# Performance work log

Measured on AMD Instinct MI355X. Metric: run time of the kernel, lower is better.

The kernel has to match this reference:

```python
import jax, jax.numpy as jnp
import numpy as np

STRIDE = 14
C_LOCAL = 2
NUM_HEADS = 12


def sparse_attention_mask(n_tokens, stride_length=STRIDE, c=C_LOCAL, mode='fixed'):
    q = jnp.arange(n_tokens)[:, None]  # row index Q
    k = jnp.arange(n_tokens)[None, :]  # col index K
    if mode == 'fixed':
        m1 = (q // stride_length) == (k // stride_length)
        m2 = ((k % stride_length) >= stride_length - c) & ((k % stride_length) <= stride_length)
        return m1 | m2
    elif mode == 'strided':
        m1 = jnp.abs(q - k) <= stride_length
        m2 = ((q - k) % stride_length) == 0
        return m1 | m2


def setup_inputs() -> dict:
    key = jax.random.key(0)
    ks = jax.random.split(key, 5)
    B, N, C = 16, 1024, 768
    return {
        'x': jax.random.normal(ks[0], (B, N, C), dtype=jnp.float32),
        'w_qkv': jax.random.normal(ks[1], (3 * C, C), dtype=jnp.float32) * (1.0 / np.sqrt(C)),
        'b_qkv': jax.random.normal(ks[2], (3 * C,), dtype=jnp.float32) * 0.02,
        'w_proj': jax.random.normal(ks[3], (C, C), dtype=jnp.float32) * (1.0 / np.sqrt(C)),
        'b_proj': jax.random.normal(ks[4], (C,), dtype=jnp.float32) * 0.02,
    }


def reference(x, w_qkv, b_qkv, w_proj, b_proj):
    B, N, C = x.shape
    H = NUM_HEADS
    D = C // H
    mask = sparse_attention_mask(N, mode='fixed')  # [N, N] bool

    # qkv projection: [B,N,3C] -> [3,B,H,N,D]
    qkv = x @ w_qkv.T + b_qkv
    qkv = qkv.reshape(B, N, 3, H, D).transpose(2, 0, 3, 1, 4)
    q, k, v = qkv[0], qkv[1], qkv[2]

    # SDPA with default scale = 1/sqrt(head_dim) and boolean attn_mask
    scale = 1.0 / jnp.sqrt(jnp.asarray(D, dtype=x.dtype))
    scores = jnp.einsum('bhnd,bhmd->bhnm', q, k) * scale
    scores = jnp.where(mask[None, None, :, :], scores, jnp.finfo(scores.dtype).min)
    attn = jax.nn.softmax(scores, axis=-1)
    out = jnp.einsum('bhnm,bhmd->bhnd', attn, v)

    # merge heads and output projection
    out = out.transpose(0, 2, 1, 3).reshape(B, N, C)
    return out @ w_proj.T + b_proj
```

## Files before the change

### kernel.cpp

```cpp
#include <hip/hip_runtime.h>
#include <stdint.h>

typedef unsigned short u16;
typedef __attribute__((ext_vector_type(8))) short bf16x8;
typedef __attribute__((ext_vector_type(4))) short s16x4;
typedef __attribute__((ext_vector_type(4))) float f32x4;

__device__ __forceinline__ u16 f2bf(float f) {
  uint32_t x = __builtin_bit_cast(uint32_t, f);
  uint32_t r = (x + 0x7fffu + ((x >> 16) & 1u)) >> 16;
  return (u16)r;
}
__device__ __forceinline__ float bf2f(u16 u) {
  return __builtin_bit_cast(float, (uint32_t)u << 16);
}

typedef __attribute__((address_space(3))) uint32_t lds_u32;
typedef const __attribute__((address_space(1))) uint32_t glb_u32;
__device__ __forceinline__ void gload_lds16(const void* g, void* l) {
  __builtin_amdgcn_global_load_lds(
      reinterpret_cast<glb_u32*>(reinterpret_cast<uintptr_t>(g)),
      reinterpret_cast<lds_u32*>(reinterpret_cast<uintptr_t>(l)),
      16, 0, 0);
}

__device__ __forceinline__ int swz(int r) { return (r & 3) ^ ((r >> 2) & 3); }

__global__ void cvt_split_kernel(const float* __restrict__ in, u16* __restrict__ hi,
                                 u16* __restrict__ lo, int n4) {
  typedef __attribute__((ext_vector_type(4))) float float4v;
  int i = blockIdx.x * 256 + threadIdx.x;
  const int stride = gridDim.x * 256;
  for (; i < n4; i += stride) {
    float4v v = *(const float4v*)(in + (size_t)i * 4);
    s16x4 hv;
#pragma unroll
    for (int j = 0; j < 4; ++j) hv[j] = (short)f2bf(v[j]);
    *(s16x4*)(hi + (size_t)i * 4) = hv;
    if (lo) {
      s16x4 lv;
#pragma unroll
      for (int j = 0; j < 4; ++j) lv[j] = (short)f2bf(v[j] - bf2f((u16)hv[j]));
      *(s16x4*)(lo + (size_t)i * 4) = lv;
    }
  }
}

template <int OUTF32>
__global__ __launch_bounds__(512, 2) void gemm_bt2(
    const u16* __restrict__ A, const u16* __restrict__ B0,
    const float* __restrict__ bias, float* __restrict__ outF, u16* __restrict__ outB,
    int Ndim, int Kdim) {
  __shared__ u16 sA[3][256 * 32];
  __shared__ u16 sB[3][256 * 32];

  const int tid = threadIdx.x;
  const int lane = tid & 63;
  const int wid = tid >> 6;
  const int wr = wid >> 2;
  const int wc = wid & 3;
  const int brow = blockIdx.x * 256;
  const int bcol = blockIdx.y * 256;
  const int colL = lane & 15;
  const int kgrp = lane >> 4;
  const int NT = Kdim >> 5;

  int srcA[2], srcB[2], ldsU[2];
#pragma unroll
  for (int j = 0; j < 2; ++j) {
    const int u = (wid * 2 + j) * 64 + lane;
    const int r = u >> 2;
    const int sl = (u & 3) ^ swz(r);
    srcA[j] = (brow + r) * Kdim + sl * 8;
    srcB[j] = (bcol + r) * Kdim + sl * 8;
    ldsU[j] = u * 8;
  }

  int oa[8], ob[4];
#pragma unroll
  for (int m = 0; m < 8; ++m) {
    const int r = wr * 128 + m * 16 + colL;
    oa[m] = r * 32 + ((kgrp ^ swz(r)) * 8);
  }
#pragma unroll
  for (int n = 0; n < 4; ++n) {
    const int r = wc * 64 + n * 16 + colL;
    ob[n] = r * 32 + ((kgrp ^ swz(r)) * 8);
  }

  auto stage = [&](int buf, int t) {
    const int k0 = t << 5;
#pragma unroll
    for (int j = 0; j < 2; ++j) {
      gload_lds16(A + (size_t)(srcA[j] + k0), &sA[buf][ldsU[j]]);
      gload_lds16(B0 + (size_t)(srcB[j] + k0), &sB[buf][ldsU[j]]);
    }
  };

  f32x4 acc[8][4] = {};

  stage(0, 0);
  stage(1, 1);
  asm volatile("s_waitcnt vmcnt(4)" ::: "memory");
  __builtin_amdgcn_s_barrier();

  for (int t = 0; t < NT; ++t) {
    const int cur = t % 3;
    if (t + 2 < NT) stage((t + 2) % 3, t + 2);

    bf16x8 a[8], b[4];
#pragma unroll
    for (int m = 0; m < 8; ++m) a[m] = *(const bf16x8*)&sA[cur][oa[m]];
#pragma unroll
    for (int n = 0; n < 4; ++n) b[n] = *(const bf16x8*)&sB[cur][ob[n]];

    __builtin_amdgcn_s_setprio(1);
#pragma unroll
    for (int m = 0; m < 8; ++m)
#pragma unroll
      for (int n = 0; n < 4; ++n)
        acc[m][n] = __builtin_amdgcn_mfma_f32_16x16x32_bf16(a[m], b[n], acc[m][n], 0, 0, 0);
    __builtin_amdgcn_s_setprio(0);

    if (t + 2 < NT)
      asm volatile("s_waitcnt vmcnt(4)" ::: "memory");
    else
      asm volatile("s_waitcnt vmcnt(0)" ::: "memory");
    __builtin_amdgcn_s_barrier();
  }

  const int r0 = kgrp * 4;
#pragma unroll
  for (int n = 0; n < 4; ++n) {
    const int colg = bcol + wc * 64 + n * 16 + colL;
    const float bv = bias[colg];
#pragma unroll
    for (int m = 0; m < 8; ++m) {
      const int rowg = brow + wr * 128 + m * 16 + r0;
#pragma unroll
      for (int r = 0; r < 4; ++r) {
        const float v = acc[m][n][r] + bv;
        if (OUTF32)
          outF[(size_t)(rowg + r) * Ndim + colg] = v;
        else
          outB[(size_t)(rowg + r) * Ndim + colg] = f2bf(v);
      }
    }
  }
}

__global__ __launch_bounds__(256) void transpose_v_kernel(const u16* __restrict__ qkv,
                                                          u16* __restrict__ vt) {
  __shared__ u16 t[64][72];
  const int tid = threadIdx.x;
  const int nt = blockIdx.x, h = blockIdx.y, b = blockIdx.z;
  const u16* src = qkv + (size_t)(b * 1024 + nt * 64) * 2304 + 1536 + h * 64;
#pragma unroll
  for (int j = 0; j < 2; ++j) {
    const int c = j * 256 + tid;
    const int row = c >> 3;
    const int off = (c & 7) * 8;
    *(bf16x8*)&t[row][off] = *(const bf16x8*)(src + (size_t)row * 2304 + off);
  }
  __syncthreads();
  u16* dst = vt + (size_t)(b * 12 + h) * 64 * 1024 + nt * 64;
#pragma unroll
  for (int j = 0; j < 2; ++j) {
    const int c = j * 256 + tid;
    const int drow = c >> 3;
    const int noff = (c & 7) * 8;
    bf16x8 o;
#pragma unroll
    for (int i = 0; i < 8; ++i) o[i] = (short)t[noff + i][drow];
    *(bf16x8*)(dst + (size_t)drow * 1024 + noff) = o;
  }
}

__global__ __launch_bounds__(256) void gather_global_kernel(const u16* __restrict__ qkv,
                                                            u16* __restrict__ kgc,
                                                            u16* __restrict__ vgc) {
  __shared__ u16 tl[192][72];
  const int tid = threadIdx.x;
  const int h = blockIdx.x % 12;
  const int b = blockIdx.x / 12;
  const u16* Kg = qkv + (size_t)(b * 1024) * 2304 + 768 + h * 64;
  const u16* Vg = qkv + (size_t)(b * 1024) * 2304 + 1536 + h * 64;
  u16* kout = kgc + (size_t)blockIdx.x * 192 * 64;
  u16* vout = vgc + (size_t)blockIdx.x * 64 * 192;

  for (int t = tid; t < 1536; t += 256) {
    const int s = t >> 3, ch = t & 7;
    bf16x8 kv = {}, vv = {};
    if (s < 146) {
      const int tok = (s >> 1) * 14 + 12 + (s & 1);
      kv = *(const bf16x8*)(Kg + (size_t)tok * 2304 + ch * 8);
      vv = *(const bf16x8*)(Vg + (size_t)tok * 2304 + ch * 8);
    }
    *(bf16x8*)(kout + s * 64 + ch * 8) = kv;
    *(bf16x8*)&tl[s][ch * 8] = vv;
  }
  __syncthreads();
  for (int t = tid; t < 64 * 24; t += 256) {
    const int d = t / 24, c8 = (t % 24) * 8;
    bf16x8 o;
#pragma unroll
    for (int i = 0; i < 8; ++i) o[i] = (short)tl[c8 + i][d];
    *(bf16x8*)(vout + (size_t)d * 192 + c8) = o;
  }
}

__global__ __launch_bounds__(256, 2) void attn_kernel(const u16* __restrict__ qkv,
                                                      const u16* __restrict__ vt,
                                                      const u16* __restrict__ kgc,
                                                      const u16* __restrict__ vgc,
                                                      u16* __restrict__ ao) {
  __shared__ u16 sQ[64 * 64];
  __shared__ u16 sK[2][64 * 64];
  __shared__ u16 sV[2][64 * 64];
  __shared__ u16 sP[4][16 * 72];

  const int tid = threadIdx.x;
  const int lane = tid & 63;
  const int wid = tid >> 6;
  const int qt = blockIdx.x, h = blockIdx.y, b = blockIdx.z;
  const int q0 = qt * 64;
  const int colL = lane & 15;
  const int kgrp = lane >> 4;
  const int bh = b * 12 + h;

  const u16* Qg = qkv + (size_t)(b * 1024 + q0) * 2304 + h * 64;
  const u16* Kg = qkv + (size_t)(b * 1024) * 2304 + 768 + h * 64;
  const u16* Vt = vt + (size_t)bh * 64 * 1024;
  const u16* Kc = kgc + (size_t)bh * 192 * 64;
  const u16* Vc = vgc + (size_t)bh * 64 * 192;

  const int first_blk = q0 / 14;
  const int tok0a = (first_blk * 14) & ~7;

  auto stage_kv = [&](int buf, int it) {
    if (it < 3) {
#pragma unroll
      for (int j = 0; j < 2; ++j) {
        const int c = j * 256 + tid;
        const int row = c >> 3;
        const int sb = ((c & 7) * 16) ^ ((row & 7) << 4);
        gload_lds16((const char*)(Kc + (size_t)(it * 64 + row) * 64) + sb, &sK[buf][c * 8]);
        gload_lds16((const char*)(Vc + (size_t)row * 192 + it * 64) + sb, &sV[buf][c * 8]);
      }
    } else {
      const int tc0 = tok0a + (it - 3) * 64;
#pragma unroll
      for (int j = 0; j < 2; ++j) {
        const int c = j * 256 + tid;
        const int row = c >> 3;
        const int sb = ((c & 7) * 16) ^ ((row & 7) << 4);
        const int ktok = min(tc0 + row, 1023);
        gload_lds16((const char*)(Kg + (size_t)ktok * 2304) + sb, &sK[buf][c * 8]);
        const int vb = min(tc0 * 2 + sb, 2032);
        gload_lds16((const char*)(Vt + (size_t)row * 1024) + vb, &sV[buf][c * 8]);
      }
    }
  };

#pragma unroll
  for (int j = 0; j < 2; ++j) {
    const int c = j * 256 + tid;
    const int row = c >> 3;
    const int off = (c & 7) * 8;
    gload_lds16(Qg + (size_t)row * 2304 + off, &sQ[c * 8]);
  }
  stage_kv(0, 0);
  __syncthreads();

  bf16x8 qf[2];
#pragma unroll
  for (int ks = 0; ks < 2; ++ks)
    qf[ks] = *(const bf16x8*)&sQ[(wid * 16 + colL) * 64 + ks * 32 + kgrp * 8];

  int qblk[4];
#pragma unroll
  for (int r = 0; r < 4; ++r) qblk[r] = (q0 + wid * 16 + kgrp * 4 + r) / 14;

  const float SCL = 0.125f * 1.44269504088896f;
  const float NEG = -3e38f;
  float mrun[4] = {NEG, NEG, NEG, NEG};
  float lsum[4] = {0.f, 0.f, 0.f, 0.f};
  f32x4 oacc[4] = {};

  for (int it = 0; it < 5; ++it) {
    const int cur = it & 1;
    if (it + 1 < 5) stage_kv(cur ^ 1, it + 1);

    f32x4 s[4] = {};
#pragma unroll
    for (int n = 0; n < 4; ++n) {
      const int row = n * 16 + colL;
#pragma unroll
      for (int ks = 0; ks < 2; ++ks) {
        const int cb = (ks * 32 + kgrp * 8) * 2;
        bf16x8 kf = *(const bf16x8*)((const char*)&sK[cur][0] + row * 128 + (cb ^ ((row & 7) << 4)));
        s[n] = __builtin_amdgcn_mfma_f32_16x16x32_bf16(qf[ks], kf, s[n], 0, 0, 0);
      }
    }

    float sv[4][4];
    if (it < 3) {
#pragma unroll
      for (int n = 0; n < 4; ++n) {
        const bool gv = (it * 64 + n * 16 + colL) < 146;
#pragma unroll
        for (int r = 0; r < 4; ++r) sv[n][r] = gv ? s[n][r] * SCL : NEG;
      }
    } else {
      const int tc0 = tok0a + (it - 3) * 64;
#pragma unroll
      for (int n = 0; n < 4; ++n) {
        const int t = tc0 + n * 16 + colL;
        const int tb = t / 14;
        const bool cv = (t < 1024) && ((t - tb * 14) < 12);
#pragma unroll
        for (int r = 0; r < 4; ++r) {
          const bool ok = cv && (tb == qblk[r]);
          sv[n][r] = ok ? s[n][r] * SCL : NEG;
        }
      }
    }

    float pmax[4];
#pragma unroll
    for (int r = 0; r < 4; ++r) {
      float v = fmaxf(fmaxf(sv[0][r], sv[1][r]), fmaxf(sv[2][r], sv[3][r]));
#pragma unroll
      for (int msk = 1; msk <= 8; msk <<= 1) v = fmaxf(v, __shfl_xor(v, msk));
      pmax[r] = v;
    }

    float corr[4], psum[4];
#pragma unroll
    for (int r = 0; r < 4; ++r) {
      const float mn = fmaxf(mrun[r], pmax[r]);
      corr[r] = exp2f(mrun[r] - mn);
      mrun[r] = mn;
      psum[r] = 0.f;
    }

    float p[4][4];
#pragma unroll
    for (int n = 0; n < 4; ++n)
#pragma unroll
      for (int r = 0; r < 4; ++r) {
        p[n][r] = exp2f(sv[n][r] - mrun[r]);
        psum[r] += p[n][r];
      }

#pragma unroll
    for (int r = 0; r < 4; ++r) {
      float v = psum[r];
#pragma unroll
      for (int msk = 1; msk <= 8; msk <<= 1) v += __shfl_xor(v, msk);
      lsum[r] = lsum[r] * corr[r] + v;
    }

#pragma unroll
    for (int n = 0; n < 4; ++n)
#pragma unroll
      for (int r = 0; r < 4; ++r)
        sP[wid][(kgrp * 4 + r) * 72 + n * 16 + colL] = f2bf(p[n][r]);

#pragma unroll
    for (int dn = 0; dn < 4; ++dn)
#pragma unroll
      for (int r = 0; r < 4; ++r) oacc[dn][r] *= corr[r];

#pragma unroll
    for (int ks = 0; ks < 2; ++ks) {
      bf16x8 pf = *(const bf16x8*)&sP[wid][colL * 72 + ks * 32 + kgrp * 8];
#pragma unroll
      for (int dn = 0; dn < 4; ++dn) {
        const int vrow = dn * 16 + colL;
        const int cb = (ks * 32 + kgrp * 8) * 2;
        bf16x8 vf = *(const bf16x8*)((const char*)&sV[cur][0] + vrow * 128 + (cb ^ ((vrow & 7) << 4)));
        oacc[dn] = __builtin_amdgcn_mfma_f32_16x16x32_bf16(pf, vf, oacc[dn], 0, 0, 0);
      }
    }

    __syncthreads();
  }

  float inv[4];
#pragma unroll
  for (int r = 0; r < 4; ++r) inv[r] = 1.0f / lsum[r];
#pragma unroll
  for (int dn = 0; dn < 4; ++dn)
#pragma unroll
    for (int r = 0; r < 4; ++r) {
      const int rowg = b * 1024 + q0 + wid * 16 + kgrp * 4 + r;
      const int colg = h * 64 + dn * 16 + colL;
      ao[(size_t)rowg * 768 + colg] = f2bf(oacc[dn][r] * inv[r]);
    }
}

extern "C" void kernel_launch(void* const* d_in, const int* in_sizes, int n_in,
                              void* d_out, int out_size, void* d_ws, size_t ws_size,
                              hipStream_t stream) {
  const float* x = (const float*)d_in[0];
  const float* w_qkv = (const float*)d_in[1];
  const float* b_qkv = (const float*)d_in[2];
  const float* w_proj = (const float*)d_in[3];
  const float* b_proj = (const float*)d_in[4];
  float* out = (float*)d_out;

  char* ws = (char*)d_ws;
  size_t off = 0;
  auto alloc = [&](size_t bytes) {
    char* p = ws + off;
    off += (bytes + 255) & ~(size_t)255;
    return p;
  };
  u16* x_bf = (u16*)alloc(16384ull * 768 * 2);
  u16* wq_bf = (u16*)alloc(2304ull * 768 * 2);
  u16* wp_bf = (u16*)alloc(768ull * 768 * 2);
  u16* qkvb = (u16*)alloc(16384ull * 2304 * 2);
  u16* vt = (u16*)alloc(192ull * 64 * 1024 * 2);
  u16* kgc = (u16*)alloc(192ull * 192 * 64 * 2);
  u16* vgc = (u16*)alloc(192ull * 64 * 192 * 2);
  u16* ao = x_bf;

  cvt_split_kernel<<<dim3(4096), dim3(256), 0, stream>>>(x, x_bf, nullptr, 16384 * 768 / 4);
  cvt_split_kernel<<<dim3(1728), dim3(256), 0, stream>>>(w_qkv, wq_bf, nullptr, 2304 * 768 / 4);
  cvt_split_kernel<<<dim3(576), dim3(256), 0, stream>>>(w_proj, wp_bf, nullptr, 768 * 768 / 4);

  gemm_bt2<0><<<dim3(64, 9), dim3(512), 0, stream>>>(x_bf, wq_bf, b_qkv,
                                                     nullptr, qkvb, 2304, 768);
  transpose_v_kernel<<<dim3(16, 12, 16), dim3(256), 0, stream>>>(qkvb, vt);
  gather_global_kernel<<<dim3(192), dim3(256), 0, stream>>>(qkvb, kgc, vgc);
  attn_kernel<<<dim3(16, 12, 16), dim3(256), 0, stream>>>(qkvb, vt, kgc, vgc, ao);
  gemm_bt2<1><<<dim3(64, 3), dim3(512), 0, stream>>>(ao, wp_bf, b_proj,
                                                     out, nullptr, 768, 768);
}
```

Measured before the change: 221.8 us.

## Restructure GEMM into 8-phase pipelined schedule with K=64 tiles and double buffering

Rewrites the bf16 GEMM main loop to use 64-wide K tiles with two LDS buffers instead of three 32-wide buffers. Each K-step is split into four quadrant phases, and the A/B prefetches for step t+2 are interleaved between MFMA blocks so global loads overlap compute. The LDS swizzle changes to an XOR over 8 slots, and launch bounds drop to one block per SM because LDS use doubles to 128KB. The extra barriers per iteration and the lower occupancy could offset the better overlap.

Result: faster. 210.8 us (-5.0%).

```diff
diff --git a/kernel.cpp b/kernel.cpp
--- a/kernel.cpp
+++ b/kernel.cpp
@@ -23,8 +23,6 @@
       reinterpret_cast<lds_u32*>(reinterpret_cast<uintptr_t>(l)),
       16, 0, 0);
 }
-
-__device__ __forceinline__ int swz(int r) { return (r & 3) ^ ((r >> 2) & 3); }
 
 __global__ void cvt_split_kernel(const float* __restrict__ in, u16* __restrict__ hi,
                                  u16* __restrict__ lo, int n4) {
@@ -47,12 +45,12 @@
 }
 
 template <int OUTF32>
-__global__ __launch_bounds__(512, 2) void gemm_bt2(
+__global__ __launch_bounds__(512, 1) void gemm_8p(
     const u16* __restrict__ A, const u16* __restrict__ B0,
     const float* __restrict__ bias, float* __restrict__ outF, u16* __restrict__ outB,
     int Ndim, int Kdim) {
-  __shared__ u16 sA[3][256 * 32];
-  __shared__ u16 sB[3][256 * 32];
+  __shared__ u16 sA[2][256 * 64];
+  __shared__ u16 sB[2][256 * 64];
 
   const int tid = threadIdx.x;
   const int lane = tid & 63;
@@ -63,70 +61,137 @@
   const int bcol = blockIdx.y * 256;
   const int colL = lane & 15;
   const int kgrp = lane >> 4;
-  const int NT = Kdim >> 5;
-
-  int srcA[2], srcB[2], ldsU[2];
-#pragma unroll
-  for (int j = 0; j < 2; ++j) {
-    const int u = (wid * 2 + j) * 64 + lane;
-    const int r = u >> 2;
-    const int sl = (u & 3) ^ swz(r);
-    srcA[j] = (brow + r) * Kdim + sl * 8;
-    srcB[j] = (bcol + r) * Kdim + sl * 8;
-    ldsU[j] = u * 8;
-  }
-
-  int oa[8], ob[4];
+  const int NT = Kdim >> 6;
+
+  int srcA[4], srcB[4], ldsOff[4];
+#pragma unroll
+  for (int j = 0; j < 4; ++j) {
+    const int u = j * 512 + tid;
+    const int r = u >> 3;
+    const int s = u & 7;
+    const int sp = (s ^ (r & 7)) * 8;
+    srcA[j] = (brow + r) * Kdim + sp;
+    srcB[j] = (bcol + r) * Kdim + sp;
+    ldsOff[j] = u * 8;
+  }
+
+  int offA[8][2], offB[4][2];
 #pragma unroll
   for (int m = 0; m < 8; ++m) {
     const int r = wr * 128 + m * 16 + colL;
-    oa[m] = r * 32 + ((kgrp ^ swz(r)) * 8);
+#pragma unroll
+    for (int kk = 0; kk < 2; ++kk)
+      offA[m][kk] = r * 64 + ((kk * 32 + kgrp * 8) ^ ((r & 7) << 3));
   }
 #pragma unroll
   for (int n = 0; n < 4; ++n) {
     const int r = wc * 64 + n * 16 + colL;
-    ob[n] = r * 32 + ((kgrp ^ swz(r)) * 8);
-  }
-
-  auto stage = [&](int buf, int t) {
-    const int k0 = t << 5;
-#pragma unroll
-    for (int j = 0; j < 2; ++j) {
-      gload_lds16(A + (size_t)(srcA[j] + k0), &sA[buf][ldsU[j]]);
-      gload_lds16(B0 + (size_t)(srcB[j] + k0), &sB[buf][ldsU[j]]);
-    }
+#pragma unroll
+    for (int kk = 0; kk < 2; ++kk)
+      offB[n][kk] = r * 64 + ((kk * 32 + kgrp * 8) ^ ((r & 7) << 3));
+  }
+
+  auto stageA = [&](int slot, int kt) {
+    const int k0 = kt << 6;
+#pragma unroll
+    for (int j = 0; j < 4; ++j)
+      gload_lds16(A + (size_t)(srcA[j] + k0), &sA[slot][ldsOff[j]]);
   };
+  auto stageB = [&](int slot, int kt) {
+    const int k0 = kt << 6;
+#pragma unroll
+    for (int j = 0; j < 4; ++j)
+      gload_lds16(B0 + (size_t)(srcB[j] + k0), &sB[slot][ldsOff[j]]);
+  };
 
   f32x4 acc[8][4] = {};
 
-  stage(0, 0);
-  stage(1, 1);
-  asm volatile("s_waitcnt vmcnt(4)" ::: "memory");
-  __builtin_amdgcn_s_barrier();
+  stageA(0, 0);
+  stageB(0, 0);
+  if (NT > 1) {
+    stageA(1, 1);
+    stageB(1, 1);
+    asm volatile("s_waitcnt vmcnt(8)" ::: "memory");
+  } else {
+    asm volatile("s_waitcnt vmcnt(0)" ::: "memory");
+  }
+  asm volatile("s_barrier" ::: "memory");
 
   for (int t = 0; t < NT; ++t) {
-    const int cur = t % 3;
-    if (t + 2 < NT) stage((t + 2) % 3, t + 2);
-
-    bf16x8 a[8], b[4];
-#pragma unroll
-    for (int m = 0; m < 8; ++m) a[m] = *(const bf16x8*)&sA[cur][oa[m]];
-#pragma unroll
-    for (int n = 0; n < 4; ++n) b[n] = *(const bf16x8*)&sB[cur][ob[n]];
-
+    const int d = t & 1;
+    bf16x8 a0[4][2], a1[4][2], b0[2][2], b1[2][2];
+
+#pragma unroll
+    for (int m = 0; m < 4; ++m)
+#pragma unroll
+      for (int kk = 0; kk < 2; ++kk) a0[m][kk] = *(const bf16x8*)&sA[d][offA[m][kk]];
+#pragma unroll
+    for (int n = 0; n < 2; ++n)
+#pragma unroll
+      for (int kk = 0; kk < 2; ++kk) b0[n][kk] = *(const bf16x8*)&sB[d][offB[n][kk]];
+    asm volatile("s_waitcnt lgkmcnt(0)" ::: "memory");
+    __builtin_amdgcn_sched_barrier(0);
     __builtin_amdgcn_s_setprio(1);
 #pragma unroll
-    for (int m = 0; m < 8; ++m)
-#pragma unroll
-      for (int n = 0; n < 4; ++n)
-        acc[m][n] = __builtin_amdgcn_mfma_f32_16x16x32_bf16(a[m], b[n], acc[m][n], 0, 0, 0);
+    for (int m = 0; m < 4; ++m)
+#pragma unroll
+      for (int n = 0; n < 2; ++n)
+#pragma unroll
+        for (int kk = 0; kk < 2; ++kk)
+          acc[m][n] = __builtin_amdgcn_mfma_f32_16x16x32_bf16(a0[m][kk], b0[n][kk], acc[m][n], 0, 0, 0);
     __builtin_amdgcn_s_setprio(0);
-
+    asm volatile("s_barrier" ::: "memory");
+
+#pragma unroll
+    for (int n = 0; n < 2; ++n)
+#pragma unroll
+      for (int kk = 0; kk < 2; ++kk) b1[n][kk] = *(const bf16x8*)&sB[d][offB[n + 2][kk]];
+    asm volatile("s_waitcnt lgkmcnt(0)" ::: "memory");
+    __builtin_amdgcn_sched_barrier(0);
+    __builtin_amdgcn_s_setprio(1);
+#pragma unroll
+    for (int m = 0; m < 4; ++m)
+#pragma unroll
+      for (int n = 0; n < 2; ++n)
+#pragma unroll
+        for (int kk = 0; kk < 2; ++kk)
+          acc[m][n + 2] = __builtin_amdgcn_mfma_f32_16x16x32_bf16(a0[m][kk], b1[n][kk], acc[m][n + 2], 0, 0, 0);
+    __builtin_amdgcn_s_setprio(0);
+    asm volatile("s_barrier" ::: "memory");
+
+#pragma unroll
+    for (int m = 0; m < 4; ++m)
+#pragma unroll
+      for (int kk = 0; kk < 2; ++kk) a1[m][kk] = *(const bf16x8*)&sA[d][offA[m + 4][kk]];
+    asm volatile("s_waitcnt lgkmcnt(0)" ::: "memory");
+    __builtin_amdgcn_sched_barrier(0);
+    if (t + 2 < NT) stageB(d, t + 2);
+    __builtin_amdgcn_s_setprio(1);
+#pragma unroll
+    for (int m = 0; m < 4; ++m)
+#pragma unroll
+      for (int n = 0; n < 2; ++n)
+#pragma unroll
+        for (int kk = 0; kk < 2; ++kk)
+          acc[m + 4][n + 2] = __builtin_amdgcn_mfma_f32_16x16x32_bf16(a1[m][kk], b1[n][kk], acc[m + 4][n + 2], 0, 0, 0);
+    __builtin_amdgcn_s_setprio(0);
+    asm volatile("s_barrier" ::: "memory");
+
+    if (t + 2 < NT) stageA(d, t + 2);
+    __builtin_amdgcn_s_setprio(1);
+#pragma unroll
+    for (int m = 0; m < 4; ++m)
+#pragma unroll
+      for (int n = 0; n < 2; ++n)
+#pragma unroll
+        for (int kk = 0; kk < 2; ++kk)
+          acc[m + 4][n] = __builtin_amdgcn_mfma_f32_16x16x32_bf16(a1[m][kk], b0[n][kk], acc[m + 4][n], 0, 0, 0);
+    __builtin_amdgcn_s_setprio(0);
     if (t + 2 < NT)
-      asm volatile("s_waitcnt vmcnt(4)" ::: "memory");
-    else
+      asm volatile("s_waitcnt vmcnt(8)" ::: "memory");
+    else if (t + 1 < NT)
       asm volatile("s_waitcnt vmcnt(0)" ::: "memory");
-    __builtin_amdgcn_s_barrier();
+    asm volatile("s_barrier" ::: "memory");
   }
 
   const int r0 = kgrp * 4;
@@ -430,11 +495,11 @@
   cvt_split_kernel<<<dim3(1728), dim3(256), 0, stream>>>(w_qkv, wq_bf, nullptr, 2304 * 768 / 4);
   cvt_split_kernel<<<dim3(576), dim3(256), 0, stream>>>(w_proj, wp_bf, nullptr, 768 * 768 / 4);
 
-  gemm_bt2<0><<<dim3(64, 9), dim3(512), 0, stream>>>(x_bf, wq_bf, b_qkv,
-                                                     nullptr, qkvb, 2304, 768);
+  gemm_8p<0><<<dim3(64, 9), dim3(512), 0, stream>>>(x_bf, wq_bf, b_qkv,
+                                                    nullptr, qkvb, 2304, 768);
   transpose_v_kernel<<<dim3(16, 12, 16), dim3(256), 0, stream>>>(qkvb, vt);
   gather_global_kernel<<<dim3(192), dim3(256), 0, stream>>>(qkvb, kgc, vgc);
   attn_kernel<<<dim3(16, 12, 16), dim3(256), 0, stream>>>(qkvb, vt, kgc, vgc, ao);
-  gemm_bt2<1><<<dim3(64, 3), dim3(512), 0, stream>>>(ao, wp_bf, b_proj,
-                                                     out, nullptr, 768, 768);
-}
+  gemm_8p<1><<<dim3(64, 3), dim3(512), 0, stream>>>(ao, wp_bf, b_proj,
+                                                    out, nullptr, 768, 768);
+}
```

## Replace GEMM tiling with full-K A-resident row-panel kernel streaming B panels

Applied to the files above, without the earlier changes.

Both projection GEMMs now use a kernel where each block loads a 64x768 slab of A fully into LDS once and streams all output-column panels of B through a triple-buffered pipeline. Results are written out after each 256-wide panel. The launch grows from 576 or 192 blocks to 256 blocks, which evens out the wave count across CUs. The intent is to avoid re-reading A for every column tile and to balance work. The cost is much larger LDS use (occupancy 1 block per CU), a smaller per-wave MFMA tile (2x4 instead of 8x4) with more B traffic, and K fixed at 768.

Result: slower. 238.4 us (+7.5%).

```diff
diff --git a/kernel.cpp b/kernel.cpp
--- a/kernel.cpp
+++ b/kernel.cpp
@@ -24,7 +24,7 @@
       16, 0, 0);
 }
 
-__device__ __forceinline__ int swz(int r) { return (r & 3) ^ ((r >> 2) & 3); }
+__device__ __forceinline__ int swzB(int r) { return (r & 3) ^ ((r >> 2) & 3); }
 
 __global__ void cvt_split_kernel(const float* __restrict__ in, u16* __restrict__ hi,
                                  u16* __restrict__ lo, int n4) {
@@ -46,12 +46,11 @@
   }
 }
 
-template <int OUTF32>
-__global__ __launch_bounds__(512, 2) void gemm_bt2(
+template <int OUTF32, int NPAN>
+__global__ __launch_bounds__(512, 1) void gemm_sn(
     const u16* __restrict__ A, const u16* __restrict__ B0,
-    const float* __restrict__ bias, float* __restrict__ outF, u16* __restrict__ outB,
-    int Ndim, int Kdim) {
-  __shared__ u16 sA[3][256 * 32];
+    const float* __restrict__ bias, float* __restrict__ outF, u16* __restrict__ outB) {
+  __shared__ u16 sA[64 * 768];
   __shared__ u16 sB[3][256 * 32];
 
   const int tid = threadIdx.x;
@@ -59,93 +58,105 @@
   const int wid = tid >> 6;
   const int wr = wid >> 2;
   const int wc = wid & 3;
-  const int brow = blockIdx.x * 256;
-  const int bcol = blockIdx.y * 256;
+  const int brow = blockIdx.x * 64;
   const int colL = lane & 15;
   const int kgrp = lane >> 4;
-  const int NT = Kdim >> 5;
-
-  int srcA[2], srcB[2], ldsU[2];
+  const int Ndim = NPAN * 256;
+  const int G = NPAN * 24;
+
+  int srcA[12];
+#pragma unroll
+  for (int j = 0; j < 12; ++j) {
+    const int u = j * 512 + tid;
+    const int r = u / 96;
+    const int s = u % 96;
+    srcA[j] = (brow + r) * 768 + ((s ^ (r & 7)) * 8);
+  }
+
+  int rowB[2], ldsB[2];
 #pragma unroll
   for (int j = 0; j < 2; ++j) {
-    const int u = (wid * 2 + j) * 64 + lane;
+    const int u = j * 512 + tid;
     const int r = u >> 2;
-    const int sl = (u & 3) ^ swz(r);
-    srcA[j] = (brow + r) * Kdim + sl * 8;
-    srcB[j] = (bcol + r) * Kdim + sl * 8;
-    ldsU[j] = u * 8;
-  }
-
-  int oa[8], ob[4];
-#pragma unroll
-  for (int m = 0; m < 8; ++m) {
-    const int r = wr * 128 + m * 16 + colL;
-    oa[m] = r * 32 + ((kgrp ^ swz(r)) * 8);
-  }
-#pragma unroll
-  for (int n = 0; n < 4; ++n) {
-    const int r = wc * 64 + n * 16 + colL;
-    ob[n] = r * 32 + ((kgrp ^ swz(r)) * 8);
-  }
-
-  auto stage = [&](int buf, int t) {
-    const int k0 = t << 5;
-#pragma unroll
-    for (int j = 0; j < 2; ++j) {
-      gload_lds16(A + (size_t)(srcA[j] + k0), &sA[buf][ldsU[j]]);
-      gload_lds16(B0 + (size_t)(srcB[j] + k0), &sB[buf][ldsU[j]]);
-    }
+    const int s = u & 3;
+    rowB[j] = r * 768 + ((s ^ swzB(r)) * 8);
+    ldsB[j] = u * 8;
+  }
+
+  const int ax = colL & 7;
+  int baseA[2];
+#pragma unroll
+  for (int m = 0; m < 2; ++m) baseA[m] = (wr * 32 + m * 16 + colL) * 768;
+  const int slotB = kgrp ^ swzB(colL);
+  int offB[4];
+#pragma unroll
+  for (int n = 0; n < 4; ++n) offB[n] = (wc * 64 + n * 16 + colL) * 32 + slotB * 8;
+
+  auto stageB = [&](int slot, int g) {
+    const int pan = g / 24, t = g % 24;
+    const int base = pan * (256 * 768) + t * 32;
+#pragma unroll
+    for (int j = 0; j < 2; ++j)
+      gload_lds16(B0 + (size_t)(rowB[j] + base), &sB[slot][ldsB[j]]);
   };
 
-  f32x4 acc[8][4] = {};
-
-  stage(0, 0);
-  stage(1, 1);
-  asm volatile("s_waitcnt vmcnt(4)" ::: "memory");
+#pragma unroll
+  for (int j = 0; j < 12; ++j)
+    gload_lds16(A + (size_t)srcA[j], &sA[(size_t)(j * 512 + tid) * 8]);
+  stageB(0, 0);
+  if (G > 1) stageB(1, 1);
+  asm volatile("s_waitcnt vmcnt(2)" ::: "memory");
   __builtin_amdgcn_s_barrier();
 
-  for (int t = 0; t < NT; ++t) {
-    const int cur = t % 3;
-    if (t + 2 < NT) stage((t + 2) % 3, t + 2);
-
-    bf16x8 a[8], b[4];
-#pragma unroll
-    for (int m = 0; m < 8; ++m) a[m] = *(const bf16x8*)&sA[cur][oa[m]];
-#pragma unroll
-    for (int n = 0; n < 4; ++n) b[n] = *(const bf16x8*)&sB[cur][ob[n]];
+  f32x4 acc[2][4] = {};
+
+  for (int g = 0; g < G; ++g) {
+    const int cur = g % 3;
+    const int t = g % 24;
+    if (g + 2 < G) stageB((g + 2) % 3, g + 2);
+
+    const int sa = ((t * 4 + kgrp) ^ ax) * 8;
+    bf16x8 a[2], b[4];
+#pragma unroll
+    for (int m = 0; m < 2; ++m) a[m] = *(const bf16x8*)&sA[baseA[m] + sa];
+#pragma unroll
+    for (int n = 0; n < 4; ++n) b[n] = *(const bf16x8*)&sB[cur][offB[n]];
 
     __builtin_amdgcn_s_setprio(1);
 #pragma unroll
-    for (int m = 0; m < 8; ++m)
+    for (int m = 0; m < 2; ++m)
 #pragma unroll
       for (int n = 0; n < 4; ++n)
         acc[m][n] = __builtin_amdgcn_mfma_f32_16x16x32_bf16(a[m], b[n], acc[m][n], 0, 0, 0);
     __builtin_amdgcn_s_setprio(0);
 
-    if (t + 2 < NT)
-      asm volatile("s_waitcnt vmcnt(4)" ::: "memory");
-    else
+    if (t == 23) {
+      const int pan = g / 24;
+#pragma unroll
+      for (int n = 0; n < 4; ++n) {
+        const int colg = pan * 256 + wc * 64 + n * 16 + colL;
+        const float bv = bias[colg];
+#pragma unroll
+        for (int m = 0; m < 2; ++m) {
+          const int rowg = brow + wr * 32 + m * 16 + kgrp * 4;
+#pragma unroll
+          for (int r = 0; r < 4; ++r) {
+            const float v = acc[m][n][r] + bv;
+            if (OUTF32)
+              outF[(size_t)(rowg + r) * Ndim + colg] = v;
+            else
+              outB[(size_t)(rowg + r) * Ndim + colg] = f2bf(v);
+            acc[m][n][r] = 0.f;
+          }
+        }
+      }
+    }
+
+    if (g + 2 < G)
+      asm volatile("s_waitcnt vmcnt(2)" ::: "memory");
+    else if (g + 1 < G)
       asm volatile("s_waitcnt vmcnt(0)" ::: "memory");
     __builtin_amdgcn_s_barrier();
-  }
-
-  const int r0 = kgrp * 4;
-#pragma unroll
-  for (int n = 0; n < 4; ++n) {
-    const int colg = bcol + wc * 64 + n * 16 + colL;
-    const float bv = bias[colg];
-#pragma unroll
-    for (int m = 0; m < 8; ++m) {
-      const int rowg = brow + wr * 128 + m * 16 + r0;
-#pragma unroll
-      for (int r = 0; r < 4; ++r) {
-        const float v = acc[m][n][r] + bv;
-        if (OUTF32)
-          outF[(size_t)(rowg + r) * Ndim + colg] = v;
-        else
-          outB[(size_t)(rowg + r) * Ndim + colg] = f2bf(v);
-      }
-    }
   }
 }
 
@@ -430,11 +441,9 @@
   cvt_split_kernel<<<dim3(1728), dim3(256), 0, stream>>>(w_qkv, wq_bf, nullptr, 2304 * 768 / 4);
   cvt_split_kernel<<<dim3(576), dim3(256), 0, stream>>>(w_proj, wp_bf, nullptr, 768 * 768 / 4);
 
-  gemm_bt2<0><<<dim3(64, 9), dim3(512), 0, stream>>>(x_bf, wq_bf, b_qkv,
-                                                     nullptr, qkvb, 2304, 768);
+  gemm_sn<0, 9><<<dim3(256), dim3(512), 0, stream>>>(x_bf, wq_bf, b_qkv, nullptr, qkvb);
   transpose_v_kernel<<<dim3(16, 12, 16), dim3(256), 0, stream>>>(qkvb, vt);
   gather_global_kernel<<<dim3(192), dim3(256), 0, stream>>>(qkvb, kgc, vgc);
   attn_kernel<<<dim3(16, 12, 16), dim3(256), 0, stream>>>(qkvb, vt, kgc, vgc, ao);
-  gemm_bt2<1><<<dim3(64, 3), dim3(512), 0, stream>>>(ao, wp_bf, b_proj,
-                                                     out, nullptr, 768, 768);
-}
+  gemm_sn<1, 3><<<dim3(256), dim3(512), 0, stream>>>(ao, wp_bf, b_proj, out, nullptr);
+}
```
